# Optimization experiments

Hardware: AMD Instinct MI355X
Metric: run time of the kernel (lower is better)

## Reference

```python
import jax, jax.numpy as jnp
import numpy as np

B, S, D = 4, 2048, 1024
HALF_PI = np.float32(np.pi / 2.0)


def setup_inputs() -> dict:
    key = jax.random.key(0)
    ks = jax.random.split(key, 12)
    std = np.float32(0.02)
    def w(k):
        return jax.random.normal(k, (D, D), dtype=jnp.float32) * std
    return {
        "x": jax.random.normal(ks[0], (B, S, D), dtype=jnp.float32),
        "W_q": w(ks[1]), "b_q": jnp.zeros((D,), jnp.float32),
        "W_k": w(ks[2]), "b_k": jnp.zeros((D,), jnp.float32),
        "W_v": w(ks[3]), "b_v": jnp.zeros((D,), jnp.float32),
        "W_t": w(ks[4]), "b_t": jnp.zeros((D,), jnp.float32),
        "W_o": w(ks[5]), "b_o": jnp.zeros((D,), jnp.float32),
        "entangle_strength": jnp.float32(0.5),
    }


def reference(x, W_q, b_q, W_k, b_k, W_v, b_v, W_t, b_t, W_o, b_o, entangle_strength):
    scale = jnp.float32(np.sqrt(D))
    Q = x @ W_q + b_q          # [B,S,D]
    K = x @ W_k + b_k
    V = x @ W_v + b_v
    # theta in [0, pi/2]; r = cos(2*theta)
    theta_q = jax.nn.sigmoid(Q @ W_t + b_t) * HALF_PI
    theta_k = jax.nn.sigmoid(K @ W_t + b_t) * HALF_PI
    r_q = jnp.cos(2.0 * theta_q)
    r_k = jnp.cos(2.0 * theta_k)
    classical = jnp.einsum("bqd,bkd->bqk", Q, K) / scale
    quantum = jnp.einsum("bqd,bkd->bqk", r_q, r_k) * entangle_strength
    attn_weights = jax.nn.softmax(classical + quantum, axis=-1)  # [B,S,S]
    # dropout: eval mode -> identity
    out = jnp.einsum("bqk,bkd->bqd", attn_weights, V)
    out = out @ W_o + b_o
    return out, attn_weights
```

## Files before the change

kernel.cpp:

```cpp
#include <hip/hip_runtime.h>
#include <cstdint>

typedef unsigned short u16;
typedef __attribute__((ext_vector_type(8))) short bf16x8;
typedef __attribute__((ext_vector_type(4))) float f32x4;

__device__ __forceinline__ u16 f2b(float x) {
  unsigned u = __float_as_uint(x);
  u += 0x7FFFu + ((u >> 16) & 1u);
  return (u16)(u >> 16);
}

__device__ __forceinline__ void gload16(const void* g, void* l) {
  __builtin_amdgcn_global_load_lds(
      (const __attribute__((address_space(1))) void*)g,
      (__attribute__((address_space(3))) void*)l, 16, 0, 0);
}

__device__ __forceinline__ int swz(int r) { return (r & 3) ^ ((r >> 2) & 3); }

__device__ __forceinline__ void stageA(const u16* __restrict__ G, int ld,
                                       int k0, u16* L, int tid) {
#pragma unroll
  for (int j = 0; j < 2; ++j) {
    const int P = j * 512 + tid;
    const int r = P >> 2;
    const int cl = (P & 3) ^ swz(r);
    gload16(G + (long long)r * ld + k0 + cl * 8, L + P * 8);
  }
}
__device__ __forceinline__ void stageB128(const u16* __restrict__ G, int ld,
                                          int k0, u16* L, int tid) {
  const int P = tid;
  const int r = P >> 2;
  const int cl = (P & 3) ^ swz(r);
  gload16(G + (long long)r * ld + k0 + cl * 8, L + P * 8);
}

template <int EPI, int NREP>
__global__ __launch_bounds__(512, 2) void g256(
    const u16* __restrict__ A, int lda, long long sAz,
    const u16* __restrict__ B, int ldb, long long sBz,
    void* __restrict__ C0, void* __restrict__ C1, void* __restrict__ C2,
    int ldc, long long sCz, int K,
    const float* __restrict__ b0, const float* __restrict__ b1,
    const float* __restrict__ b2, float preScale, const float* __restrict__ esp) {
  constexpr int BN = NREP * 64;
  constexpr int ASZ = 8192;
  constexpr int BSZ = NREP * 2048;
  constexpr int BUF = ASZ + BSZ;
  __shared__ __align__(16) u16 lds[4 * BUF];

  const int z = blockIdx.z;
  const long long tM = (long long)blockIdx.y * 256;
  const long long tN = (long long)blockIdx.x * BN;
  const u16* Ab = A + z * sAz + tM * lda;
  const u16* Bb = B + z * sBz + tN * ldb;
  const int tid = threadIdx.x;
  const int NT = K >> 5;

#pragma unroll
  for (int t = 0; t < 3; ++t) {
    u16* Lb = lds + t * BUF;
    stageA(Ab, lda, t * 32, Lb, tid);
    if constexpr (NREP == 4) stageA(Bb, ldb, t * 32, Lb + ASZ, tid);
    else stageB128(Bb, ldb, t * 32, Lb + ASZ, tid);
  }

  f32x4 acc[8][NREP] = {};
  const int wid = tid >> 6, lane = tid & 63;
  const int wr = (wid >> 2) * 128;
  const int wc = (wid & 3) * (BN / 4);
  const int lr = lane & 15;
  const int cA = lane >> 4;

  for (int t = 0; t < NT; ++t) {
    if (t < NT - 2) {
      if constexpr (NREP == 4) asm volatile("s_waitcnt vmcnt(8)" ::: "memory");
      else                     asm volatile("s_waitcnt vmcnt(6)" ::: "memory");
    } else if (t == NT - 2) {
      if constexpr (NREP == 4) asm volatile("s_waitcnt vmcnt(4)" ::: "memory");
      else                     asm volatile("s_waitcnt vmcnt(3)" ::: "memory");
    } else {
      asm volatile("s_waitcnt vmcnt(0)" ::: "memory");
    }
    __builtin_amdgcn_s_barrier();
    if (t + 3 < NT) {
      u16* Lb = lds + ((t + 3) & 3) * BUF;
      stageA(Ab, lda, (t + 3) * 32, Lb, tid);
      if constexpr (NREP == 4) stageA(Bb, ldb, (t + 3) * 32, Lb + ASZ, tid);
      else stageB128(Bb, ldb, (t + 3) * 32, Lb + ASZ, tid);
    }
    const u16* LAp = lds + (t & 3) * BUF;
    const u16* LBp = LAp + ASZ;
    bf16x8 af[8], bfr[NREP];
#pragma unroll
    for (int m = 0; m < 8; ++m) {
      const int R = wr + m * 16 + lr;
      af[m] = *(const bf16x8*)(LAp + R * 32 + ((cA ^ swz(R)) << 3));
    }
#pragma unroll
    for (int n = 0; n < NREP; ++n) {
      const int R = wc + n * 16 + lr;
      bfr[n] = *(const bf16x8*)(LBp + R * 32 + ((cA ^ swz(R)) << 3));
    }
    __builtin_amdgcn_s_setprio(1);
#pragma unroll
    for (int m = 0; m < 8; ++m)
#pragma unroll
      for (int n = 0; n < NREP; ++n)
        acc[m][n] = __builtin_amdgcn_mfma_f32_16x16x32_bf16(af[m], bfr[n],
                                                            acc[m][n], 0, 0, 0);
    __builtin_amdgcn_s_setprio(0);
  }

  const int rr = (lane >> 4) << 2;
  float ps = preScale, mul = 1.0f;
  if constexpr (EPI == 1) {
    ps = (z == 0) ? preScale : 1.0f;
    mul = (z == 0) ? esp[0] : 1.0f;
  }
#pragma unroll
  for (int m = 0; m < 8; ++m) {
#pragma unroll
    for (int n = 0; n < NREP; ++n) {
      const int col = (int)tN + wc + n * 16 + lr;
#pragma unroll
      for (int r = 0; r < 4; ++r) {
        const long long row = tM + wr + m * 16 + rr + r;
        const float v = acc[m][n][r];
        if constexpr (EPI == 0) {
          const int g = col >> 10, cc = col & 1023;
          if (g == 0)      ((u16*)C0)[row * 2048 + cc] = f2b((v + b0[cc]) * 0.03125f);
          else if (g == 1) ((u16*)C1)[row * 2048 + cc] = f2b(v + b1[cc]);
          else             ((u16*)C2)[row * 1024 + cc] = f2b(v + b2[cc]);
        } else if constexpr (EPI == 1) {
          const float tt = v * ps + b0[col];
          const float sg = 1.f / (1.f + __expf(-tt));
          ((u16*)C0)[z * sCz + row * ldc + col] = f2b(mul * cospif(sg));
        } else if constexpr (EPI == 2) {
          ((u16*)C0)[z * sCz + row * ldc + col] = f2b(v);
        } else if constexpr (EPI == 3) {
          ((float*)C0)[z * sCz + row * ldc + col] = v + b0[col];
        } else {
          ((float*)C0)[z * sCz + row * ldc + col] = v;
        }
      }
    }
  }
}

__global__ __launch_bounds__(256) void softmax_rows(float* __restrict__ L,
                                                    u16* __restrict__ AB) {
  const long long row = blockIdx.x;
  float4* p4 = (float4*)(L + row * 2048);
  const int tid = threadIdx.x;
  float4 a = p4[tid], b = p4[tid + 256];
  float m = fmaxf(fmaxf(fmaxf(a.x, a.y), fmaxf(a.z, a.w)),
                  fmaxf(fmaxf(b.x, b.y), fmaxf(b.z, b.w)));
#pragma unroll
  for (int o = 32; o > 0; o >>= 1) m = fmaxf(m, __shfl_xor(m, o));
  __shared__ float rmax[4], rsum[4];
  const int wid = tid >> 6, lane = tid & 63;
  if (lane == 0) rmax[wid] = m;
  __syncthreads();
  m = fmaxf(fmaxf(rmax[0], rmax[1]), fmaxf(rmax[2], rmax[3]));
  a.x = __expf(a.x - m); a.y = __expf(a.y - m);
  a.z = __expf(a.z - m); a.w = __expf(a.w - m);
  b.x = __expf(b.x - m); b.y = __expf(b.y - m);
  b.z = __expf(b.z - m); b.w = __expf(b.w - m);
  float s = a.x + a.y + a.z + a.w + b.x + b.y + b.z + b.w;
#pragma unroll
  for (int o = 32; o > 0; o >>= 1) s += __shfl_xor(s, o);
  if (lane == 0) rsum[wid] = s;
  __syncthreads();
  s = rsum[0] + rsum[1] + rsum[2] + rsum[3];
  const float inv = 1.0f / s;
  a.x *= inv; a.y *= inv; a.z *= inv; a.w *= inv;
  b.x *= inv; b.y *= inv; b.z *= inv; b.w *= inv;
  p4[tid] = a;
  p4[tid + 256] = b;
  ushort4* o4 = (ushort4*)(AB + row * 2048);
  o4[tid]       = make_ushort4(f2b(a.x), f2b(a.y), f2b(a.z), f2b(a.w));
  o4[tid + 256] = make_ushort4(f2b(b.x), f2b(b.y), f2b(b.z), f2b(b.w));
}

__global__ __launch_bounds__(256) void cvt_x(const float* __restrict__ X,
                                             u16* __restrict__ XB) {
  const int i = blockIdx.x * 256 + threadIdx.x;
  float4 v = ((const float4*)X)[i];
  ((ushort4*)XB)[i] = make_ushort4(f2b(v.x), f2b(v.y), f2b(v.z), f2b(v.w));
}

__global__ void cvt_w(const float* __restrict__ W0, const float* __restrict__ W1,
                      const float* __restrict__ W2, const float* __restrict__ W3,
                      const float* __restrict__ W4, u16* __restrict__ WT) {
  __shared__ float t[32][33];
  const int z = blockIdx.z;
  const float* W = (z == 0) ? W0 : (z == 1) ? W1 : (z == 2) ? W2 : (z == 3) ? W3 : W4;
  u16* D = WT + (long long)z * 1024 * 1024;
  const int c0 = blockIdx.x * 32, r0 = blockIdx.y * 32;
  const int tx = threadIdx.x, ty = threadIdx.y;
#pragma unroll
  for (int i = 0; i < 4; ++i)
    t[ty + i * 8][tx] = W[(long long)(r0 + ty + i * 8) * 1024 + c0 + tx];
  __syncthreads();
#pragma unroll
  for (int i = 0; i < 4; ++i)
    D[(long long)(c0 + ty + i * 8) * 1024 + r0 + tx] = f2b(t[tx][ty + i * 8]);
}

__global__ void transpose_v(const u16* __restrict__ Vb, u16* __restrict__ VT) {
  __shared__ u16 t[32][33];
  const int b = blockIdx.z;
  const u16* V = Vb + (long long)b * 2048 * 1024;
  u16* O = VT + (long long)b * 1024 * 2048;
  const int d0 = blockIdx.x * 32, s0 = blockIdx.y * 32;
  const int tx = threadIdx.x, ty = threadIdx.y;
#pragma unroll
  for (int i = 0; i < 4; ++i)
    t[ty + i * 8][tx] = V[(long long)(s0 + ty + i * 8) * 1024 + d0 + tx];
  __syncthreads();
#pragma unroll
  for (int i = 0; i < 4; ++i)
    O[(long long)(d0 + ty + i * 8) * 2048 + s0 + tx] = t[tx][ty + i * 8];
}

extern "C" void kernel_launch(void* const* d_in, const int* in_sizes, int n_in,
                              void* d_out, int out_size, void* d_ws,
                              size_t ws_size, hipStream_t stream) {
  const float* x  = (const float*)d_in[0];
  const float* Wq = (const float*)d_in[1];
  const float* bq = (const float*)d_in[2];
  const float* Wk = (const float*)d_in[3];
  const float* bk = (const float*)d_in[4];
  const float* Wv = (const float*)d_in[5];
  const float* bv = (const float*)d_in[6];
  const float* Wt = (const float*)d_in[7];
  const float* bt = (const float*)d_in[8];
  const float* Wo = (const float*)d_in[9];
  const float* bo = (const float*)d_in[10];
  const float* es = (const float*)d_in[11];

  char* ws = (char*)d_ws;
  u16* WT   = (u16*)(ws);
  u16* XB   = (u16*)(ws + 10485760);
  u16* Qcat = (u16*)(ws + 27262976);
  u16* Kcat = Qcat + 16777216;
  u16* Vb   = (u16*)(ws + 94371840);
  u16* VT   = (u16*)(ws + 111149056);
  u16* WtT  = WT + 3 * 1048576;
  u16* WoT  = WT + 4 * 1048576;
  u16* ATT  = Qcat;
  u16* AV   = XB;

  float* outO = (float*)d_out;
  float* outA = outO + 8388608;

  cvt_x<<<8192, 256, 0, stream>>>(x, XB);
  cvt_w<<<dim3(32, 32, 5), dim3(32, 8), 0, stream>>>(Wq, Wk, Wv, Wt, Wo, WT);
  g256<0, 4><<<dim3(12, 32, 1), 512, 0, stream>>>(
      XB, 1024, 0, WT, 1024, 0, Qcat, Kcat, Vb, 0, 0, 1024, bq, bk, bv, 1.f, nullptr);
  g256<1, 4><<<dim3(4, 32, 2), 512, 0, stream>>>(
      Qcat, 2048, 16777216LL, WtT, 1024, 0, Qcat + 1024, nullptr, nullptr,
      2048, 16777216LL, 1024, bt, nullptr, nullptr, 32.f, es);
  transpose_v<<<dim3(32, 64, 4), dim3(32, 8), 0, stream>>>(Vb, VT);
  g256<4, 4><<<dim3(8, 8, 4), 512, 0, stream>>>(
      Qcat, 2048, 4194304LL, Kcat, 2048, 4194304LL, outA, nullptr, nullptr,
      2048, 4194304LL, 2048, nullptr, nullptr, nullptr, 1.f, nullptr);
  softmax_rows<<<8192, 256, 0, stream>>>(outA, ATT);
  g256<2, 2><<<dim3(8, 8, 4), 512, 0, stream>>>(
      ATT, 2048, 4194304LL, VT, 2048, 2097152LL, AV, nullptr, nullptr,
      1024, 2097152LL, 2048, nullptr, nullptr, nullptr, 1.f, nullptr);
  g256<3, 2><<<dim3(8, 32, 1), 512, 0, stream>>>(
      AV, 1024, 0, WoT, 1024, 0, outO, nullptr, nullptr,
      1024, 0, 1024, bo, nullptr, nullptr, 1.f, nullptr);
}
```

Before: 364.1 us.

## Replace GEMM kernel with 8-phase double-buffered pipeline and XCD-aware tile swizzle

Replaces the 4-stage, single-phase GEMM main loop with a double-buffered loop over K=64 tiles. Each tile is split into four sub-phases that interleave LDS fragment reads, global-to-LDS loads for future tiles, and MFMA bursts, separated by barriers. Warp layout and tile shapes become templates (128x256 or 256x256 tiles), and the block index is remapped so that consecutive tiles are spread across the 8 XCDs for better L2 locality. The aim is to overlap memory with compute more finely and to reduce LDS footprint. In exchange it adds many more barriers per iteration and changes grid sizes.

Result: slower. 372.1 us (+2.2%).

```diff
diff --git a/kernel.cpp b/kernel.cpp
--- a/kernel.cpp
+++ b/kernel.cpp
@@ -19,99 +19,154 @@
 
 __device__ __forceinline__ int swz(int r) { return (r & 3) ^ ((r >> 2) & 3); }
 
-__device__ __forceinline__ void stageA(const u16* __restrict__ G, int ld,
-                                       int k0, u16* L, int tid) {
-#pragma unroll
-  for (int j = 0; j < 2; ++j) {
+template <int N>
+__device__ __forceinline__ void vmwait() {
+  if constexpr (N == 0) asm volatile("s_waitcnt vmcnt(0)" ::: "memory");
+  else if constexpr (N == 3) asm volatile("s_waitcnt vmcnt(3)" ::: "memory");
+  else if constexpr (N == 4) asm volatile("s_waitcnt vmcnt(4)" ::: "memory");
+  else if constexpr (N == 6) asm volatile("s_waitcnt vmcnt(6)" ::: "memory");
+  else if constexpr (N == 8) asm volatile("s_waitcnt vmcnt(8)" ::: "memory");
+}
+
+template <int L>
+__device__ __forceinline__ void stage_region(const u16* __restrict__ G,
+                                             long long ld, int gcol,
+                                             u16* L_, int tid) {
+#pragma unroll
+  for (int j = 0; j < L; ++j) {
     const int P = j * 512 + tid;
     const int r = P >> 2;
     const int cl = (P & 3) ^ swz(r);
-    gload16(G + (long long)r * ld + k0 + cl * 8, L + P * 8);
+    gload16(G + (long long)r * ld + gcol + cl * 8, L_ + P * 8);
   }
 }
-__device__ __forceinline__ void stageB128(const u16* __restrict__ G, int ld,
-                                          int k0, u16* L, int tid) {
-  const int P = tid;
-  const int r = P >> 2;
-  const int cl = (P & 3) ^ swz(r);
-  gload16(G + (long long)r * ld + k0 + cl * 8, L + P * 8);
-}
-
-template <int EPI, int NREP>
-__global__ __launch_bounds__(512, 2) void g256(
-    const u16* __restrict__ A, int lda, long long sAz,
-    const u16* __restrict__ B, int ldb, long long sBz,
+
+__device__ __forceinline__ bf16x8 frag(const u16* reg_, int row, int cA) {
+  return *(const bf16x8*)(reg_ + row * 32 + ((cA ^ swz(row)) << 3));
+}
+
+template <int EPI, int WM, int WN, int MR, int NR>
+__global__ __launch_bounds__(512, 2) void g8p(
+    const u16* __restrict__ A, long long lda, long long sAz,
+    const u16* __restrict__ B, long long ldb, long long sBz,
     void* __restrict__ C0, void* __restrict__ C1, void* __restrict__ C2,
-    int ldc, long long sCz, int K,
+    long long ldc, long long sCz, int K,
     const float* __restrict__ b0, const float* __restrict__ b1,
     const float* __restrict__ b2, float preScale, const float* __restrict__ esp) {
-  constexpr int BN = NREP * 64;
-  constexpr int ASZ = 8192;
-  constexpr int BSZ = NREP * 2048;
-  constexpr int BUF = ASZ + BSZ;
-  __shared__ __align__(16) u16 lds[4 * BUF];
-
+  constexpr int BM = WM * MR * 16, BN = WN * NR * 16;
+  constexpr int LA = BM / 128, LB = BN / 128;
+  constexpr int AHALF = BM * 32;
+  constexpr int BHALF = BN * 32;
+  constexpr int BUFU = 2 * (AHALF + BHALF);
+  constexpr int NH = NR / 2;
+  __shared__ __align__(16) u16 lds[2 * BUFU];
+
+  const int gx = gridDim.x, S = gx * gridDim.y;
+  const int hw = blockIdx.y * gx + blockIdx.x;
+  const int l = (hw & 7) * (S >> 3) + (hw >> 3);
+  const int bx = l % gx, by = l / gx;
   const int z = blockIdx.z;
-  const long long tM = (long long)blockIdx.y * 256;
-  const long long tN = (long long)blockIdx.x * BN;
+  const long long tM = (long long)by * BM;
+  const long long tN = (long long)bx * BN;
   const u16* Ab = A + z * sAz + tM * lda;
   const u16* Bb = B + z * sBz + tN * ldb;
   const int tid = threadIdx.x;
-  const int NT = K >> 5;
-
-#pragma unroll
-  for (int t = 0; t < 3; ++t) {
-    u16* Lb = lds + t * BUF;
-    stageA(Ab, lda, t * 32, Lb, tid);
-    if constexpr (NREP == 4) stageA(Bb, ldb, t * 32, Lb + ASZ, tid);
-    else stageB128(Bb, ldb, t * 32, Lb + ASZ, tid);
-  }
-
-  f32x4 acc[8][NREP] = {};
+  const int NT = K >> 6;
+
+  stage_region<LA>(Ab, lda, 0,  lds, tid);
+  stage_region<LB>(Bb, ldb, 0,  lds + 2 * AHALF, tid);
+  stage_region<LA>(Ab, lda, 32, lds + AHALF, tid);
+  stage_region<LB>(Bb, ldb, 32, lds + 2 * AHALF + BHALF, tid);
+  stage_region<LA>(Ab, lda, 64, lds + BUFU, tid);
+  stage_region<LB>(Bb, ldb, 64, lds + BUFU + 2 * AHALF, tid);
+  vmwait<2 * (LA + LB)>();
+  __builtin_amdgcn_s_barrier();
+
   const int wid = tid >> 6, lane = tid & 63;
-  const int wr = (wid >> 2) * 128;
-  const int wc = (wid & 3) * (BN / 4);
-  const int lr = lane & 15;
-  const int cA = lane >> 4;
+  const int wm = wid / WN, wn = wid % WN;
+  const int wr = wm * MR * 16, wc = wn * NR * 16;
+  const int lr = lane & 15, cA = lane >> 4;
+  f32x4 acc[MR][NR] = {};
 
   for (int t = 0; t < NT; ++t) {
-    if (t < NT - 2) {
-      if constexpr (NREP == 4) asm volatile("s_waitcnt vmcnt(8)" ::: "memory");
-      else                     asm volatile("s_waitcnt vmcnt(6)" ::: "memory");
-    } else if (t == NT - 2) {
-      if constexpr (NREP == 4) asm volatile("s_waitcnt vmcnt(4)" ::: "memory");
-      else                     asm volatile("s_waitcnt vmcnt(3)" ::: "memory");
-    } else {
-      asm volatile("s_waitcnt vmcnt(0)" ::: "memory");
-    }
-    __builtin_amdgcn_s_barrier();
-    if (t + 3 < NT) {
-      u16* Lb = lds + ((t + 3) & 3) * BUF;
-      stageA(Ab, lda, (t + 3) * 32, Lb, tid);
-      if constexpr (NREP == 4) stageA(Bb, ldb, (t + 3) * 32, Lb + ASZ, tid);
-      else stageB128(Bb, ldb, (t + 3) * 32, Lb + ASZ, tid);
-    }
-    const u16* LAp = lds + (t & 3) * BUF;
-    const u16* LBp = LAp + ASZ;
-    bf16x8 af[8], bfr[NREP];
-#pragma unroll
-    for (int m = 0; m < 8; ++m) {
-      const int R = wr + m * 16 + lr;
-      af[m] = *(const bf16x8*)(LAp + R * 32 + ((cA ^ swz(R)) << 3));
-    }
-#pragma unroll
-    for (int n = 0; n < NREP; ++n) {
-      const int R = wc + n * 16 + lr;
-      bfr[n] = *(const bf16x8*)(LBp + R * 32 + ((cA ^ swz(R)) << 3));
-    }
+    u16* bufc = lds + (t & 1) * BUFU;
+    u16* bufn = lds + ((t + 1) & 1) * BUFU;
+    const u16* Ak0p = bufc;
+    const u16* Ak1p = bufc + AHALF;
+    const u16* Bk0p = bufc + 2 * AHALF;
+    const u16* Bk1p = bufc + 2 * AHALF + BHALF;
+    bf16x8 a[MR], b[NH];
+
+#pragma unroll
+    for (int m = 0; m < MR; ++m) a[m] = frag(Ak0p, wr + m * 16 + lr, cA);
+#pragma unroll
+    for (int n = 0; n < NH; ++n) b[n] = frag(Bk0p, wc + n * 16 + lr, cA);
+    if (t + 1 < NT)
+      stage_region<LA>(Ab, lda, (t + 1) * 64 + 32, bufn + AHALF, tid);
+    __builtin_amdgcn_s_barrier();
+    asm volatile("s_waitcnt lgkmcnt(0)" ::: "memory");
     __builtin_amdgcn_s_setprio(1);
 #pragma unroll
-    for (int m = 0; m < 8; ++m)
-#pragma unroll
-      for (int n = 0; n < NREP; ++n)
-        acc[m][n] = __builtin_amdgcn_mfma_f32_16x16x32_bf16(af[m], bfr[n],
+    for (int m = 0; m < MR; ++m)
+#pragma unroll
+      for (int n = 0; n < NH; ++n)
+        acc[m][n] = __builtin_amdgcn_mfma_f32_16x16x32_bf16(a[m], b[n],
                                                             acc[m][n], 0, 0, 0);
     __builtin_amdgcn_s_setprio(0);
+    __builtin_amdgcn_s_barrier();
+
+#pragma unroll
+    for (int n = 0; n < NH; ++n) b[n] = frag(Bk0p, wc + (NH + n) * 16 + lr, cA);
+    if (t + 1 < NT)
+      stage_region<LB>(Bb, ldb, (t + 1) * 64 + 32, bufn + 2 * AHALF + BHALF, tid);
+    if (t < NT - 1) vmwait<2 * (LA + LB)>(); else vmwait<0>();
+    __builtin_amdgcn_s_barrier();
+    asm volatile("s_waitcnt lgkmcnt(0)" ::: "memory");
+    __builtin_amdgcn_s_setprio(1);
+#pragma unroll
+    for (int m = 0; m < MR; ++m)
+#pragma unroll
+      for (int n = 0; n < NH; ++n)
+        acc[m][NH + n] = __builtin_amdgcn_mfma_f32_16x16x32_bf16(
+            a[m], b[n], acc[m][NH + n], 0, 0, 0);
+    __builtin_amdgcn_s_setprio(0);
+    __builtin_amdgcn_s_barrier();
+
+#pragma unroll
+    for (int m = 0; m < MR; ++m) a[m] = frag(Ak1p, wr + m * 16 + lr, cA);
+#pragma unroll
+    for (int n = 0; n < NH; ++n) b[n] = frag(Bk1p, wc + n * 16 + lr, cA);
+    if (t + 2 < NT)
+      stage_region<LA>(Ab, lda, (t + 2) * 64, bufc, tid);
+    __builtin_amdgcn_s_barrier();
+    asm volatile("s_waitcnt lgkmcnt(0)" ::: "memory");
+    __builtin_amdgcn_s_setprio(1);
+#pragma unroll
+    for (int m = 0; m < MR; ++m)
+#pragma unroll
+      for (int n = 0; n < NH; ++n)
+        acc[m][n] = __builtin_amdgcn_mfma_f32_16x16x32_bf16(a[m], b[n],
+                                                            acc[m][n], 0, 0, 0);
+    __builtin_amdgcn_s_setprio(0);
+    __builtin_amdgcn_s_barrier();
+
+#pragma unroll
+    for (int n = 0; n < NH; ++n) b[n] = frag(Bk1p, wc + (NH + n) * 16 + lr, cA);
+    if (t + 2 < NT)
+      stage_region<LB>(Bb, ldb, (t + 2) * 64, bufc + 2 * AHALF, tid);
+    if (t < NT - 2) vmwait<2 * (LA + LB)>();
+    else if (t == NT - 2) vmwait<LA + LB>();
+    __builtin_amdgcn_s_barrier();
+    asm volatile("s_waitcnt lgkmcnt(0)" ::: "memory");
+    __builtin_amdgcn_s_setprio(1);
+#pragma unroll
+    for (int m = 0; m < MR; ++m)
+#pragma unroll
+      for (int n = 0; n < NH; ++n)
+        acc[m][NH + n] = __builtin_amdgcn_mfma_f32_16x16x32_bf16(
+            a[m], b[n], acc[m][NH + n], 0, 0, 0);
+    __builtin_amdgcn_s_setprio(0);
+    __builtin_amdgcn_s_barrier();
   }
 
   const int rr = (lane >> 4) << 2;
@@ -121,9 +176,9 @@
     mul = (z == 0) ? esp[0] : 1.0f;
   }
 #pragma unroll
-  for (int m = 0; m < 8; ++m) {
-#pragma unroll
-    for (int n = 0; n < NREP; ++n) {
+  for (int m = 0; m < MR; ++m) {
+#pragma unroll
+    for (int n = 0; n < NR; ++n) {
       const int col = (int)tN + wc + n * 16 + lr;
 #pragma unroll
       for (int r = 0; r < 4; ++r) {
@@ -259,20 +314,20 @@
 
   cvt_x<<<8192, 256, 0, stream>>>(x, XB);
   cvt_w<<<dim3(32, 32, 5), dim3(32, 8), 0, stream>>>(Wq, Wk, Wv, Wt, Wo, WT);
-  g256<0, 4><<<dim3(12, 32, 1), 512, 0, stream>>>(
+  g8p<0, 4, 2, 2, 8><<<dim3(12, 64, 1), 512, 0, stream>>>(
       XB, 1024, 0, WT, 1024, 0, Qcat, Kcat, Vb, 0, 0, 1024, bq, bk, bv, 1.f, nullptr);
-  g256<1, 4><<<dim3(4, 32, 2), 512, 0, stream>>>(
+  g8p<1, 4, 2, 2, 8><<<dim3(4, 64, 2), 512, 0, stream>>>(
       Qcat, 2048, 16777216LL, WtT, 1024, 0, Qcat + 1024, nullptr, nullptr,
       2048, 16777216LL, 1024, bt, nullptr, nullptr, 32.f, es);
   transpose_v<<<dim3(32, 64, 4), dim3(32, 8), 0, stream>>>(Vb, VT);
-  g256<4, 4><<<dim3(8, 8, 4), 512, 0, stream>>>(
+  g8p<4, 2, 4, 8, 4><<<dim3(8, 8, 4), 512, 0, stream>>>(
       Qcat, 2048, 4194304LL, Kcat, 2048, 4194304LL, outA, nullptr, nullptr,
       2048, 4194304LL, 2048, nullptr, nullptr, nullptr, 1.f, nullptr);
   softmax_rows<<<8192, 256, 0, stream>>>(outA, ATT);
-  g256<2, 2><<<dim3(8, 8, 4), 512, 0, stream>>>(
+  g8p<2, 4, 2, 2, 8><<<dim3(4, 16, 4), 512, 0, stream>>>(
       ATT, 2048, 4194304LL, VT, 2048, 2097152LL, AV, nullptr, nullptr,
       1024, 2097152LL, 2048, nullptr, nullptr, nullptr, 1.f, nullptr);
-  g256<3, 2><<<dim3(8, 32, 1), 512, 0, stream>>>(
+  g8p<3, 4, 2, 2, 8><<<dim3(4, 64, 1), 512, 0, stream>>>(
       AV, 1024, 0, WoT, 1024, 0, outO, nullptr, nullptr,
       1024, 0, 1024, bo, nullptr, nullptr, 1.f, nullptr);
 }
```

## Rework GEMM to 32x32 MFMA, 64-wide K tiles, double buffering and grouped tile order

Applied to the files above, without the earlier changes.

Replaces the 16x16x32 MFMA GEMM with a 32x32x16 variant using 64-element K tiles and an 8-chunk XOR LDS swizzle. The 4-stage async pipeline is reduced to a simple double buffer with a full wait per step. Block indices are remapped in groups to improve L2 reuse, and per-GEMM tile widths are retuned. The larger MFMA cuts LDS fragment traffic per flop, but the shallower pipeline may expose global load latency.

New measurement: 355.7 us. -2.3%, faster.

```diff
diff --git a/kernel.cpp b/kernel.cpp
--- a/kernel.cpp
+++ b/kernel.cpp
@@ -3,7 +3,7 @@
 
 typedef unsigned short u16;
 typedef __attribute__((ext_vector_type(8))) short bf16x8;
-typedef __attribute__((ext_vector_type(4))) float f32x4;
+typedef __attribute__((ext_vector_type(16))) float f32x16;
 
 __device__ __forceinline__ u16 f2b(float x) {
   unsigned u = __float_as_uint(x);
@@ -17,123 +17,121 @@
       (__attribute__((address_space(3))) void*)l, 16, 0, 0);
 }
 
-__device__ __forceinline__ int swz(int r) { return (r & 3) ^ ((r >> 2) & 3); }
-
-__device__ __forceinline__ void stageA(const u16* __restrict__ G, int ld,
-                                       int k0, u16* L, int tid) {
-#pragma unroll
-  for (int j = 0; j < 2; ++j) {
+__device__ __forceinline__ void vmwait0() {
+  asm volatile("s_waitcnt vmcnt(0)" ::: "memory");
+}
+
+template <int L>
+__device__ __forceinline__ void stage_half(const u16* __restrict__ G,
+                                           long long ld, int kb,
+                                           u16* Ldst, int tid) {
+#pragma unroll
+  for (int j = 0; j < L; ++j) {
     const int P = j * 512 + tid;
-    const int r = P >> 2;
-    const int cl = (P & 3) ^ swz(r);
-    gload16(G + (long long)r * ld + k0 + cl * 8, L + P * 8);
-  }
-}
-__device__ __forceinline__ void stageB128(const u16* __restrict__ G, int ld,
-                                          int k0, u16* L, int tid) {
-  const int P = tid;
-  const int r = P >> 2;
-  const int cl = (P & 3) ^ swz(r);
-  gload16(G + (long long)r * ld + k0 + cl * 8, L + P * 8);
-}
-
-template <int EPI, int NREP>
-__global__ __launch_bounds__(512, 2) void g256(
-    const u16* __restrict__ A, int lda, long long sAz,
-    const u16* __restrict__ B, int ldb, long long sBz,
+    const int r = P >> 3, c = P & 7;
+    gload16(G + (long long)r * ld + kb + ((c ^ (r & 7)) << 3), Ldst + P * 8);
+  }
+}
+
+__device__ __forceinline__ bf16x8 fr8(const u16* R, int row, int chunk) {
+  return *(const bf16x8*)(R + row * 64 + ((chunk ^ (row & 7)) << 3));
+}
+
+template <int EPI, int NF>
+__global__ __launch_bounds__(512, 2) void g32(
+    const u16* __restrict__ A, long long lda, long long sAz,
+    const u16* __restrict__ B, long long ldb, long long sBz,
     void* __restrict__ C0, void* __restrict__ C1, void* __restrict__ C2,
-    int ldc, long long sCz, int K,
+    long long ldc, long long sCz, int K,
     const float* __restrict__ b0, const float* __restrict__ b1,
     const float* __restrict__ b2, float preScale, const float* __restrict__ esp) {
-  constexpr int BN = NREP * 64;
-  constexpr int ASZ = 8192;
-  constexpr int BSZ = NREP * 2048;
-  constexpr int BUF = ASZ + BSZ;
-  __shared__ __align__(16) u16 lds[4 * BUF];
-
+  constexpr int BN = NF * 128;
+  constexpr int AH = 8192;
+  constexpr int BH = NF * 4096;
+  constexpr int BUFU = 2 * AH + 2 * BH;
+  __shared__ __align__(16) u16 lds[2 * BUFU];
+
+  const int gx = gridDim.x, S = gx * gridDim.y;
+  const int hw = blockIdx.y * gx + blockIdx.x;
+  const int l = (hw & 7) * (S >> 3) + (hw >> 3);
+  const int bx = l % gx, by = l / gx;
   const int z = blockIdx.z;
-  const long long tM = (long long)blockIdx.y * 256;
-  const long long tN = (long long)blockIdx.x * BN;
-  const u16* Ab = A + z * sAz + tM * lda;
-  const u16* Bb = B + z * sBz + tN * ldb;
+  const long long tM = (long long)by * 256;
+  const long long tN = (long long)bx * BN;
+  const u16* GA = A + z * sAz + tM * lda;
+  const u16* GB = B + z * sBz + tN * ldb;
   const int tid = threadIdx.x;
-  const int NT = K >> 5;
-
-#pragma unroll
-  for (int t = 0; t < 3; ++t) {
-    u16* Lb = lds + t * BUF;
-    stageA(Ab, lda, t * 32, Lb, tid);
-    if constexpr (NREP == 4) stageA(Bb, ldb, t * 32, Lb + ASZ, tid);
-    else stageB128(Bb, ldb, t * 32, Lb + ASZ, tid);
-  }
-
-  f32x4 acc[8][NREP] = {};
+  const int NT = K >> 6;
+
+  stage_half<4>(GA, lda, 0, lds, tid);
+  stage_half<2 * NF>(GB, ldb, 0, lds + 2 * AH, tid);
+  vmwait0();
+  __builtin_amdgcn_s_barrier();
+
   const int wid = tid >> 6, lane = tid & 63;
-  const int wr = (wid >> 2) * 128;
-  const int wc = (wid & 3) * (BN / 4);
-  const int lr = lane & 15;
-  const int cA = lane >> 4;
+  const int wm = wid >> 2, wn = wid & 3;
+  const int l31 = lane & 31, hk = lane >> 5;
+  f32x16 acc[4][NF] = {};
 
   for (int t = 0; t < NT; ++t) {
-    if (t < NT - 2) {
-      if constexpr (NREP == 4) asm volatile("s_waitcnt vmcnt(8)" ::: "memory");
-      else                     asm volatile("s_waitcnt vmcnt(6)" ::: "memory");
-    } else if (t == NT - 2) {
-      if constexpr (NREP == 4) asm volatile("s_waitcnt vmcnt(4)" ::: "memory");
-      else                     asm volatile("s_waitcnt vmcnt(3)" ::: "memory");
-    } else {
-      asm volatile("s_waitcnt vmcnt(0)" ::: "memory");
+    u16* cur = lds + (t & 1) * BUFU;
+    u16* oth = lds + ((t + 1) & 1) * BUFU;
+    if (t + 1 < NT) {
+      stage_half<4>(GA, lda, (t + 1) * 64, oth, tid);
+      stage_half<2 * NF>(GB, ldb, (t + 1) * 64, oth + 2 * AH, tid);
     }
+    const u16* Ahp = cur + wm * AH;
+    const u16* Bhp = cur + 2 * AH + (wn >> 1) * BH;
+    const int bbase = (wn & 1) * NF * 32;
+    bf16x8 a[4][2], b[NF][2];
+#pragma unroll
+    for (int kp = 0; kp < 2; ++kp) {
+#pragma unroll
+      for (int mf = 0; mf < 4; ++mf) {
+        a[mf][0] = fr8(Ahp, mf * 32 + l31, 4 * kp + hk);
+        a[mf][1] = fr8(Ahp, mf * 32 + l31, 4 * kp + 2 + hk);
+      }
+#pragma unroll
+      for (int nf = 0; nf < NF; ++nf) {
+        b[nf][0] = fr8(Bhp, bbase + nf * 32 + l31, 4 * kp + hk);
+        b[nf][1] = fr8(Bhp, bbase + nf * 32 + l31, 4 * kp + 2 + hk);
+      }
+      __builtin_amdgcn_s_setprio(1);
+#pragma unroll
+      for (int s = 0; s < 2; ++s)
+#pragma unroll
+        for (int mf = 0; mf < 4; ++mf)
+#pragma unroll
+          for (int nf = 0; nf < NF; ++nf)
+            acc[mf][nf] = __builtin_amdgcn_mfma_f32_32x32x16_bf16(
+                a[mf][s], b[nf][s], acc[mf][nf], 0, 0, 0);
+      __builtin_amdgcn_s_setprio(0);
+    }
+    if (t + 1 < NT) vmwait0();
     __builtin_amdgcn_s_barrier();
-    if (t + 3 < NT) {
-      u16* Lb = lds + ((t + 3) & 3) * BUF;
-      stageA(Ab, lda, (t + 3) * 32, Lb, tid);
-      if constexpr (NREP == 4) stageA(Bb, ldb, (t + 3) * 32, Lb + ASZ, tid);
-      else stageB128(Bb, ldb, (t + 3) * 32, Lb + ASZ, tid);
-    }
-    const u16* LAp = lds + (t & 3) * BUF;
-    const u16* LBp = LAp + ASZ;
-    bf16x8 af[8], bfr[NREP];
-#pragma unroll
-    for (int m = 0; m < 8; ++m) {
-      const int R = wr + m * 16 + lr;
-      af[m] = *(const bf16x8*)(LAp + R * 32 + ((cA ^ swz(R)) << 3));
-    }
-#pragma unroll
-    for (int n = 0; n < NREP; ++n) {
-      const int R = wc + n * 16 + lr;
-      bfr[n] = *(const bf16x8*)(LBp + R * 32 + ((cA ^ swz(R)) << 3));
-    }
-    __builtin_amdgcn_s_setprio(1);
-#pragma unroll
-    for (int m = 0; m < 8; ++m)
-#pragma unroll
-      for (int n = 0; n < NREP; ++n)
-        acc[m][n] = __builtin_amdgcn_mfma_f32_16x16x32_bf16(af[m], bfr[n],
-                                                            acc[m][n], 0, 0, 0);
-    __builtin_amdgcn_s_setprio(0);
-  }
-
-  const int rr = (lane >> 4) << 2;
+  }
+
   float ps = preScale, mul = 1.0f;
   if constexpr (EPI == 1) {
     ps = (z == 0) ? preScale : 1.0f;
     mul = (z == 0) ? esp[0] : 1.0f;
   }
 #pragma unroll
-  for (int m = 0; m < 8; ++m) {
-#pragma unroll
-    for (int n = 0; n < NREP; ++n) {
-      const int col = (int)tN + wc + n * 16 + lr;
-#pragma unroll
-      for (int r = 0; r < 4; ++r) {
-        const long long row = tM + wr + m * 16 + rr + r;
-        const float v = acc[m][n][r];
+  for (int mf = 0; mf < 4; ++mf) {
+#pragma unroll
+    for (int nf = 0; nf < NF; ++nf) {
+      const int col = (int)tN + wn * NF * 32 + nf * 32 + l31;
+      const f32x16 vv = acc[mf][nf];
+#pragma unroll
+      for (int reg = 0; reg < 16; ++reg) {
+        const long long row =
+            tM + wm * 128 + mf * 32 + (reg & 3) + 8 * (reg >> 2) + 4 * hk;
+        const float v = vv[reg];
         if constexpr (EPI == 0) {
-          const int g = col >> 10, cc = col & 1023;
-          if (g == 0)      ((u16*)C0)[row * 2048 + cc] = f2b((v + b0[cc]) * 0.03125f);
-          else if (g == 1) ((u16*)C1)[row * 2048 + cc] = f2b(v + b1[cc]);
-          else             ((u16*)C2)[row * 1024 + cc] = f2b(v + b2[cc]);
+          const int gg = col >> 10, cc = col & 1023;
+          if (gg == 0)      ((u16*)C0)[row * 2048 + cc] = f2b((v + b0[cc]) * 0.03125f);
+          else if (gg == 1) ((u16*)C1)[row * 2048 + cc] = f2b(v + b1[cc]);
+          else              ((u16*)C2)[row * 1024 + cc] = f2b(v + b2[cc]);
         } else if constexpr (EPI == 1) {
           const float tt = v * ps + b0[col];
           const float sg = 1.f / (1.f + __expf(-tt));
@@ -259,20 +257,21 @@
 
   cvt_x<<<8192, 256, 0, stream>>>(x, XB);
   cvt_w<<<dim3(32, 32, 5), dim3(32, 8), 0, stream>>>(Wq, Wk, Wv, Wt, Wo, WT);
-  g256<0, 4><<<dim3(12, 32, 1), 512, 0, stream>>>(
-      XB, 1024, 0, WT, 1024, 0, Qcat, Kcat, Vb, 0, 0, 1024, bq, bk, bv, 1.f, nullptr);
-  g256<1, 4><<<dim3(4, 32, 2), 512, 0, stream>>>(
+  g32<0, 1><<<dim3(24, 32, 1), 512, 0, stream>>>(
+      XB, 1024, 0, WT, 1024, 0, Qcat, Kcat, Vb, 0, 0, 1024, bq, bk, bv,
+      1.f, nullptr);
+  g32<1, 2><<<dim3(4, 32, 2), 512, 0, stream>>>(
       Qcat, 2048, 16777216LL, WtT, 1024, 0, Qcat + 1024, nullptr, nullptr,
       2048, 16777216LL, 1024, bt, nullptr, nullptr, 32.f, es);
   transpose_v<<<dim3(32, 64, 4), dim3(32, 8), 0, stream>>>(Vb, VT);
-  g256<4, 4><<<dim3(8, 8, 4), 512, 0, stream>>>(
+  g32<4, 2><<<dim3(8, 8, 4), 512, 0, stream>>>(
       Qcat, 2048, 4194304LL, Kcat, 2048, 4194304LL, outA, nullptr, nullptr,
       2048, 4194304LL, 2048, nullptr, nullptr, nullptr, 1.f, nullptr);
   softmax_rows<<<8192, 256, 0, stream>>>(outA, ATT);
-  g256<2, 2><<<dim3(8, 8, 4), 512, 0, stream>>>(
+  g32<2, 1><<<dim3(8, 8, 4), 512, 0, stream>>>(
       ATT, 2048, 4194304LL, VT, 2048, 2097152LL, AV, nullptr, nullptr,
       1024, 2097152LL, 2048, nullptr, nullptr, nullptr, 1.f, nullptr);
-  g256<3, 2><<<dim3(8, 32, 1), 512, 0, stream>>>(
+  g32<3, 1><<<dim3(8, 32, 1), 512, 0, stream>>>(
       AV, 1024, 0, WoT, 1024, 0, outO, nullptr, nullptr,
       1024, 0, 1024, bo, nullptr, nullptr, 1.f, nullptr);
 }
```
